# Optimization experiments

Measured on AMD Instinct MI355X. Metric: run time of the kernel, lower is better.

The kernel has to match this reference:

```python
import jax, jax.numpy as jnp
import numpy as np

B, S, D, H, DFF = 8, 1024, 1024, 16, 4096
DK = D // H
NEG = -1000000000.0


def layernorm(x, g, b, eps=1e-5):
    mu = jnp.mean(x, axis=-1, keepdims=True)
    var = jnp.mean((x - mu) ** 2, axis=-1, keepdims=True)
    return (x - mu) / jnp.sqrt(var + eps) * g + b


def setup_inputs() -> dict:
    key = jax.random.key(0)
    ks = jax.random.split(key, 16)
    s = 0.02
    inp = {
        "x": jax.random.normal(ks[0], (B, S, D), jnp.float32),
        "binary_mask": jax.random.randint(ks[1], (B, S), 0, 2, jnp.int32),
        # per-head projections stacked: [H, D, DK]
        "Wq": jax.random.normal(ks[2], (H, D, DK), jnp.float32) * s,
        "bq": jnp.zeros((H, DK), jnp.float32),
        "Wk": jax.random.normal(ks[3], (H, D, DK), jnp.float32) * s,
        "bk": jnp.zeros((H, DK), jnp.float32),
        "Wv": jax.random.normal(ks[4], (H, D, DK), jnp.float32) * s,
        "bv": jnp.zeros((H, DK), jnp.float32),
        "Wo": jax.random.normal(ks[5], (D, D), jnp.float32) * s,
        "bo": jnp.zeros((D,), jnp.float32),
        "ga": jnp.ones((D,), jnp.float32),
        "ba": jnp.zeros((D,), jnp.float32),
        "W1": jax.random.normal(ks[6], (D, DFF), jnp.float32) * s,
        "b1": jnp.zeros((DFF,), jnp.float32),
        "W2": jax.random.normal(ks[7], (DFF, D), jnp.float32) * s,
        "b2": jnp.zeros((D,), jnp.float32),
        "gf": jnp.ones((D,), jnp.float32),
        "bf": jnp.zeros((D,), jnp.float32),
    }
    return inp


def encoder_fwd(x, binary_mask, Wq, bq, Wk, bk, Wv, bv, Wo, bo, ga, ba, W1, b1, W2, b2, gf, bf):
    # --- multi-head self-attention (heads vectorized over h axis) ---
    q = jnp.einsum("bsd,hdk->bhsk", x, Wq) + bq[None, :, None, :]
    k = jnp.einsum("bsd,hdk->bhsk", x, Wk) + bk[None, :, None, :]
    v = jnp.einsum("bsd,hdk->bhsk", x, Wv) + bv[None, :, None, :]
    score = jnp.einsum("bhik,bhjk->bhij", q, k) / jnp.sqrt(jnp.float32(DK))
    # mask: binary_mask is over KEY positions, broadcast over query dim
    score = score + jnp.where(binary_mask[:, None, None, :] == 0, NEG, 0.0)
    # NOTE: original code softmaxes over dim=1 of [B,Sq,Sk] -> the QUERY axis
    probs = jax.nn.softmax(score, axis=2)
    ctx = jnp.einsum("bhij,bhjk->bhik", probs, v)  # [B,H,S,DK]
    ctx = jnp.transpose(ctx, (0, 2, 1, 3)).reshape(x.shape[0], x.shape[1], D)
    attn_out = ctx @ Wo + bo
    y = layernorm(x + attn_out, ga, ba)
    # --- FFN ---
    h = jax.nn.relu(y @ W1 + b1)
    ffn_out = h @ W2 + b2
    return layernorm(y + ffn_out, gf, bf)


def reference(x, binary_mask, Wq, bq, Wk, bk, Wv, bv, Wo, bo, ga, ba, W1, b1, W2, b2, gf, bf):
    return encoder_fwd(x, binary_mask, Wq, bq, Wk, bk, Wv, bv, Wo, bo, ga, ba, W1, b1, W2, b2, gf, bf)
```

## Files before the change

kernel.cpp:

```cpp
#include <hip/hip_runtime.h>
#include <hip/hip_bf16.h>

typedef __bf16 bf16;
typedef __bf16 bf16x8 __attribute__((ext_vector_type(8)));
typedef __bf16 bf16x4 __attribute__((ext_vector_type(4)));
typedef float  f32x4  __attribute__((ext_vector_type(4)));

#define NB 8
#define NS 1024
#define ND 1024
#define NH 16
#define NDK 64
#define NDFF 4096
#define LDT 72
#define LDP 40

static __device__ __forceinline__ f32x4 mfma16(bf16x8 a, bf16x8 b, f32x4 c) {
    return __builtin_amdgcn_mfma_f32_16x16x32_bf16(a, b, c, 0, 0, 0);
}

#define GLDS(g, l) __builtin_amdgcn_global_load_lds( \
    (const __attribute__((address_space(1))) void*)(g), \
    (__attribute__((address_space(3))) void*)(l), 16, 0, 0)

__global__ __launch_bounds__(256) void cvt_x(const float* __restrict__ in,
                                             bf16* __restrict__ out, int n4)
{
    int idx = blockIdx.x * 256 + threadIdx.x;
    if (idx >= n4) return;
    float4 v = ((const float4*)in)[idx];
    bf16x4 o = { (bf16)v.x, (bf16)v.y, (bf16)v.z, (bf16)v.w };
    ((bf16x4*)out)[idx] = o;
}

__global__ __launch_bounds__(256) void prep_transpose(
    const float* __restrict__ Wq, const float* __restrict__ Wk, const float* __restrict__ Wv,
    const float* __restrict__ Wo, const float* __restrict__ W1, const float* __restrict__ W2,
    bf16* __restrict__ wqkvT, bf16* __restrict__ WoT,
    bf16* __restrict__ W1T, bf16* __restrict__ W2T)
{
    __shared__ float T[64][65];
    int bid = blockIdx.x;
    const float* src; bf16* dst; int srcLd, dstLd, tR, tC; bool scale = false;
    if (bid < 768) {
        int mat = bid >> 4, ty = bid & 15;
        int h = mat & 15, type = mat >> 4;
        const float* W = (type == 0) ? Wq : (type == 1 ? Wk : Wv);
        src = W + (size_t)h * ND * NDK;
        srcLd = NDK; tR = ty * 64; tC = 0;
        dst = wqkvT + ((size_t)type * 1024 + h * 64) * ND;
        dstLd = ND;
        scale = (type == 0);
    } else if (bid < 1024) {
        int b2 = bid - 768; int ty = b2 >> 4, tx = b2 & 15;
        src = Wo; srcLd = ND; tR = ty * 64; tC = tx * 64; dst = WoT; dstLd = ND;
    } else if (bid < 2048) {
        int b2 = bid - 1024; int ty = b2 >> 6, tx = b2 & 63;
        src = W1; srcLd = NDFF; tR = ty * 64; tC = tx * 64; dst = W1T; dstLd = ND;
    } else {
        int b2 = bid - 2048; int ty = b2 >> 4, tx = b2 & 15;
        src = W2; srcLd = ND; tR = ty * 64; tC = tx * 64; dst = W2T; dstLd = NDFF;
    }
    int t = threadIdx.x;
    int c0 = t & 63, r0 = t >> 6;
    #pragma unroll
    for (int rr = 0; rr < 16; rr++) {
        int row = rr * 4 + r0;
        T[row][c0] = src[(size_t)(tR + row) * srcLd + tC + c0];
    }
    __syncthreads();
    #pragma unroll
    for (int cc = 0; cc < 16; cc++) {
        int col = cc * 4 + r0;
        float v = T[c0][col];
        if (scale) v *= 0.125f;
        dst[(size_t)(tC + col) * dstLd + tR + c0] = (bf16)v;
    }
}

__global__ void prep_bias(const float* __restrict__ bq, const float* __restrict__ bk,
                          const float* __restrict__ bv, float* __restrict__ bqkv)
{
    int n = blockIdx.x * 256 + threadIdx.x;
    if (n >= 3072) return;
    int type = n >> 10, hk = n & 1023;
    const float* bb = (type == 0) ? bq : (type == 1 ? bk : bv);
    float v = bb[hk];
    if (type == 0) v *= 0.125f;
    bqkv[n] = v;
}

__device__ __forceinline__ void gemm_bt_core(
    const bf16* __restrict__ A, const bf16* __restrict__ BT, int K,
    int rowBase, int colBase, f32x4 (&acc)[4][4], bf16* As, bf16* Bs)
{
    const int tid = threadIdx.x;
    const int lane = tid & 63, wid = tid >> 6;
    const int wr = (wid >> 1) * 64, wc = (wid & 1) * 64;
    const int lrow = lane & 15, lq = lane >> 4;
    const int srow = wid * 32 + (lane >> 3);
    const int gblk = (lane & 7) ^ ((lane >> 3) & 7);
    const bf16* Arow = A + (size_t)(rowBase + srow) * K + gblk * 8;
    const bf16* Brow = BT + (size_t)(colBase + srow) * K + gblk * 8;
    const int co0 = ((lq) ^ (lrow & 7)) * 8;
    const int co1 = ((4 + lq) ^ (lrow & 7)) * 8;
    f32x4 zz = {0.f, 0.f, 0.f, 0.f};
    #pragma unroll
    for (int i = 0; i < 4; i++)
        #pragma unroll
        for (int j = 0; j < 4; j++) acc[i][j] = zz;
    for (int k0 = 0; k0 < K; k0 += 64) {
        __syncthreads();
        #pragma unroll
        for (int it = 0; it < 4; it++)
            GLDS(Arow + (size_t)it * 8 * K + k0, As + (wid * 32 + it * 8) * 64);
        #pragma unroll
        for (int it = 0; it < 4; it++)
            GLDS(Brow + (size_t)it * 8 * K + k0, Bs + (wid * 32 + it * 8) * 64);
        __syncthreads();
        #pragma unroll
        for (int kh = 0; kh < 2; kh++) {
            const int co = kh ? co1 : co0;
            bf16x8 af[4], bfr[4];
            #pragma unroll
            for (int tt = 0; tt < 4; tt++) {
                af[tt]  = *(const bf16x8*)&As[(wr + tt * 16 + lrow) * 64 + co];
                bfr[tt] = *(const bf16x8*)&Bs[(wc + tt * 16 + lrow) * 64 + co];
            }
            #pragma unroll
            for (int i = 0; i < 4; i++)
                #pragma unroll
                for (int j = 0; j < 4; j++)
                    acc[i][j] = mfma16(af[i], bfr[j], acc[i][j]);
        }
    }
}

__global__ __launch_bounds__(256) void g1_qkv(
    const bf16* __restrict__ x, const bf16* __restrict__ wqkvT, const float* __restrict__ bqkv,
    bf16* __restrict__ Q, bf16* __restrict__ Kb, bf16* __restrict__ Vt)
{
    __shared__ bf16 As[128 * 64], Bs[128 * 64];
    f32x4 acc[4][4];
    int rowBase = blockIdx.x * 128, colBase = blockIdx.y * 128;
    gemm_bt_core(x, wqkvT, ND, rowBase, colBase, acc, As, Bs);
    const int tid = threadIdx.x, lane = tid & 63, wid = tid >> 6;
    const int wr = (wid >> 1) * 64, wc = (wid & 1) * 64, lrow = lane & 15, lq = lane >> 4;
    #pragma unroll
    for (int j = 0; j < 4; j++) {
        int gcol = colBase + wc + j * 16 + lrow;
        float bias = bqkv[gcol];
        int type = gcol >> 10, h = (gcol >> 6) & 15, kk = gcol & 63;
        #pragma unroll
        for (int i = 0; i < 4; i++) {
            #pragma unroll
            for (int r = 0; r < 4; r++) {
                int grow = rowBase + wr + i * 16 + lq * 4 + r;
                int b = grow >> 10, s = grow & 1023;
                int bh = b * NH + h;
                bf16 val = (bf16)(acc[i][j][r] + bias);
                if (type == 0)      Q [((size_t)bh * NS + s) * NDK + kk] = val;
                else if (type == 1) Kb[((size_t)bh * NS + s) * NDK + kk] = val;
                else                Vt[((size_t)bh * NDK + kk) * NS + s] = val;
            }
        }
    }
}

__global__ __launch_bounds__(256) void g2_stats(
    const bf16* __restrict__ Q, const bf16* __restrict__ Kb,
    const int* __restrict__ mask, float* __restrict__ alpha)
{
    __shared__ bf16 Ks[128 * LDT];
    __shared__ bf16 Qs[32 * LDT];
    int bh = blockIdx.y, b = bh >> 4;
    int jBase = blockIdx.x * 128;
    const bf16* Kp = Kb + (size_t)bh * NS * NDK;
    const bf16* Qp = Q + (size_t)bh * NS * NDK;
    const int tid = threadIdx.x, lane = tid & 63, wid = tid >> 6;
    const int lrow = lane & 15, lq = lane >> 4, wj = wid * 32;
    #pragma unroll
    for (int c = 0; c < 4; c++) {
        int g = tid + c * 256, row = g >> 3, kc = (g & 7) * 8;
        *(bf16x8*)&Ks[row * LDT + kc] = *(const bf16x8*)&Kp[(size_t)(jBase + row) * NDK + kc];
    }
    float Lacc[2][4];
    #pragma unroll
    for (int jt = 0; jt < 2; jt++)
        #pragma unroll
        for (int r = 0; r < 4; r++) Lacc[jt][r] = 0.f;
    for (int i0 = 0; i0 < NS; i0 += 32) {
        __syncthreads();
        {
            int row = tid >> 3, kc = (tid & 7) * 8;
            *(bf16x8*)&Qs[row * LDT + kc] = *(const bf16x8*)&Qp[(size_t)(i0 + row) * NDK + kc];
        }
        __syncthreads();
        bf16x8 af[2][2], bq8[2][2];
        #pragma unroll
        for (int jt = 0; jt < 2; jt++)
            #pragma unroll
            for (int kh = 0; kh < 2; kh++)
                af[jt][kh] = *(const bf16x8*)&Ks[(wj + jt * 16 + lrow) * LDT + kh * 32 + lq * 8];
        #pragma unroll
        for (int it = 0; it < 2; it++)
            #pragma unroll
            for (int kh = 0; kh < 2; kh++)
                bq8[it][kh] = *(const bf16x8*)&Qs[(it * 16 + lrow) * LDT + kh * 32 + lq * 8];
        #pragma unroll
        for (int jt = 0; jt < 2; jt++) {
            #pragma unroll
            for (int it = 0; it < 2; it++) {
                f32x4 s = {0.f, 0.f, 0.f, 0.f};
                s = mfma16(af[jt][0], bq8[it][0], s);
                s = mfma16(af[jt][1], bq8[it][1], s);
                #pragma unroll
                for (int r = 0; r < 4; r++) Lacc[jt][r] += __expf(s[r]);
            }
        }
    }
    #pragma unroll
    for (int jt = 0; jt < 2; jt++) {
        #pragma unroll
        for (int r = 0; r < 4; r++) {
            float v = Lacc[jt][r];
            v += __shfl_xor(v, 1); v += __shfl_xor(v, 2);
            v += __shfl_xor(v, 4); v += __shfl_xor(v, 8);
            if (lrow == 0) {
                int j = jBase + wj + jt * 16 + lq * 4 + r;
                alpha[(size_t)bh * NS + j] = mask[b * NS + j] ? 1.f / v : 0.f;
            }
        }
    }
}

__global__ __launch_bounds__(256) void kc_cmask(
    const bf16* __restrict__ Vt, const int* __restrict__ mask, float* __restrict__ cmask)
{
    int bh = blockIdx.x, b = bh >> 4;
    int tid = threadIdx.x;
    int kk = tid & 63, part = tid >> 6;
    const bf16* vrow = Vt + ((size_t)bh * NDK + kk) * NS;
    float s = 0.f;
    for (int j = part * 256; j < part * 256 + 256; j++)
        if (mask[b * NS + j] == 0) s += (float)vrow[j];
    __shared__ float red[256];
    red[tid] = s;
    __syncthreads();
    if (part == 0) {
        float t = red[kk] + red[kk + 64] + red[kk + 128] + red[kk + 192];
        cmask[bh * NDK + kk] = t * (1.f / 1024.f);
    }
}

__global__ __launch_bounds__(256) void g3_ctx(
    const bf16* __restrict__ Q, const bf16* __restrict__ Kb, const bf16* __restrict__ Vt,
    const float* __restrict__ alpha, const float* __restrict__ cmask, bf16* __restrict__ ctx)
{
    __shared__ bf16 Qs[128 * LDT];
    __shared__ bf16 Ks[32 * LDT];
    __shared__ bf16 Vs[64 * LDP];
    __shared__ bf16 Ps[4 * 32 * LDP];
    int bh = blockIdx.y, iBase = blockIdx.x * 128;
    int b = bh >> 4, h = bh & 15;
    const bf16* Qp = Q + (size_t)bh * NS * NDK;
    const bf16* Kp = Kb + (size_t)bh * NS * NDK;
    const bf16* Vp = Vt + (size_t)bh * NDK * NS;
    const float* al = alpha + (size_t)bh * NS;
    const int tid = threadIdx.x, lane = tid & 63, wid = tid >> 6;
    const int lrow = lane & 15, lq = lane >> 4, wi = wid * 32;
    #pragma unroll
    for (int c = 0; c < 4; c++) {
        int g = tid + c * 256, row = g >> 3, kc = (g & 7) * 8;
        *(bf16x8*)&Qs[row * LDT + kc] = *(const bf16x8*)&Qp[(size_t)(iBase + row) * NDK + kc];
    }
    f32x4 cacc[2][4];
    f32x4 zz = {0.f, 0.f, 0.f, 0.f};
    #pragma unroll
    for (int it = 0; it < 2; it++)
        #pragma unroll
        for (int kt = 0; kt < 4; kt++) cacc[it][kt] = zz;
    bf16* Pw = Ps + wid * 32 * LDP;
    for (int j0 = 0; j0 < NS; j0 += 32) {
        __syncthreads();
        {
            int row = tid >> 3, kc = (tid & 7) * 8;
            *(bf16x8*)&Ks[row * LDT + kc] = *(const bf16x8*)&Kp[(size_t)(j0 + row) * NDK + kc];
        }
        {
            int kk = tid >> 2, ch = (tid & 3) * 8;
            *(bf16x8*)&Vs[kk * LDP + ch] = *(const bf16x8*)&Vp[(size_t)kk * NS + j0 + ch];
        }
        __syncthreads();
        bf16x8 qa[2][2], kb8[2][2];
        #pragma unroll
        for (int it = 0; it < 2; it++)
            #pragma unroll
            for (int kh = 0; kh < 2; kh++)
                qa[it][kh] = *(const bf16x8*)&Qs[(wi + it * 16 + lrow) * LDT + kh * 32 + lq * 8];
        #pragma unroll
        for (int jt = 0; jt < 2; jt++)
            #pragma unroll
            for (int kh = 0; kh < 2; kh++)
                kb8[jt][kh] = *(const bf16x8*)&Ks[(jt * 16 + lrow) * LDT + kh * 32 + lq * 8];
        float aj0 = al[j0 + lrow];
        float aj1 = al[j0 + 16 + lrow];
        #pragma unroll
        for (int it = 0; it < 2; it++) {
            #pragma unroll
            for (int jt = 0; jt < 2; jt++) {
                f32x4 s = {0.f, 0.f, 0.f, 0.f};
                s = mfma16(qa[it][0], kb8[jt][0], s);
                s = mfma16(qa[it][1], kb8[jt][1], s);
                float aj = jt ? aj1 : aj0;
                #pragma unroll
                for (int r = 0; r < 4; r++) {
                    float p = aj * __expf(s[r]);
                    Pw[(it * 16 + lq * 4 + r) * LDP + jt * 16 + lrow] = (bf16)p;
                }
            }
        }
        __syncthreads();
        bf16x8 pa[2], vb[4];
        #pragma unroll
        for (int it = 0; it < 2; it++)
            pa[it] = *(const bf16x8*)&Pw[(it * 16 + lrow) * LDP + lq * 8];
        #pragma unroll
        for (int kt = 0; kt < 4; kt++)
            vb[kt] = *(const bf16x8*)&Vs[(kt * 16 + lrow) * LDP + lq * 8];
        #pragma unroll
        for (int it = 0; it < 2; it++)
            #pragma unroll
            for (int kt = 0; kt < 4; kt++)
                cacc[it][kt] = mfma16(pa[it], vb[kt], cacc[it][kt]);
    }
    #pragma unroll
    for (int kt = 0; kt < 4; kt++) {
        float cm = cmask[bh * NDK + kt * 16 + lrow];
        int col = h * NDK + kt * 16 + lrow;
        #pragma unroll
        for (int it = 0; it < 2; it++) {
            #pragma unroll
            for (int r = 0; r < 4; r++) {
                int i = iBase + wi + it * 16 + lq * 4 + r;
                ctx[(size_t)(b * NS + i) * ND + col] = (bf16)(cacc[it][kt][r] + cm);
            }
        }
    }
}

__global__ __launch_bounds__(256) void g4_proj(
    const bf16* __restrict__ ctx, const bf16* __restrict__ WoT, const float* __restrict__ bo,
    const float* __restrict__ x, float* __restrict__ t1f)
{
    __shared__ bf16 As[128 * 64], Bs[128 * 64];
    f32x4 acc[4][4];
    int rowBase = blockIdx.x * 128, colBase = blockIdx.y * 128;
    gemm_bt_core(ctx, WoT, ND, rowBase, colBase, acc, As, Bs);
    const int tid = threadIdx.x, lane = tid & 63, wid = tid >> 6;
    const int wr = (wid >> 1) * 64, wc = (wid & 1) * 64, lrow = lane & 15, lq = lane >> 4;
    #pragma unroll
    for (int j = 0; j < 4; j++) {
        int gcol = colBase + wc + j * 16 + lrow;
        float bias = bo[gcol];
        #pragma unroll
        for (int i = 0; i < 4; i++) {
            #pragma unroll
            for (int r = 0; r < 4; r++) {
                int grow = rowBase + wr + i * 16 + lq * 4 + r;
                float v = acc[i][j][r] + bias + x[(size_t)grow * ND + gcol];
                t1f[(size_t)grow * ND + gcol] = v;
            }
        }
    }
}

__global__ __launch_bounds__(256) void g5_ffn1(
    const bf16* __restrict__ y, const bf16* __restrict__ W1T, const float* __restrict__ b1,
    bf16* __restrict__ hb)
{
    __shared__ bf16 As[128 * 64], Bs[128 * 64];
    f32x4 acc[4][4];
    int rowBase = blockIdx.x * 128, colBase = blockIdx.y * 128;
    gemm_bt_core(y, W1T, ND, rowBase, colBase, acc, As, Bs);
    const int tid = threadIdx.x, lane = tid & 63, wid = tid >> 6;
    const int wr = (wid >> 1) * 64, wc = (wid & 1) * 64, lrow = lane & 15, lq = lane >> 4;
    #pragma unroll
    for (int j = 0; j < 4; j++) {
        int gcol = colBase + wc + j * 16 + lrow;
        float bias = b1[gcol];
        #pragma unroll
        for (int i = 0; i < 4; i++) {
            #pragma unroll
            for (int r = 0; r < 4; r++) {
                int grow = rowBase + wr + i * 16 + lq * 4 + r;
                float v = fmaxf(acc[i][j][r] + bias, 0.f);
                hb[(size_t)grow * NDFF + gcol] = (bf16)v;
            }
        }
    }
}

__global__ __launch_bounds__(256) void g6_ffn2(
    const bf16* __restrict__ hb, const bf16* __restrict__ W2T, const float* __restrict__ b2,
    const float* __restrict__ yf, float* __restrict__ zf)
{
    __shared__ bf16 As[128 * 64], Bs[128 * 64];
    f32x4 acc[4][4];
    int rowBase = blockIdx.x * 128, colBase = blockIdx.y * 128;
    gemm_bt_core(hb, W2T, NDFF, rowBase, colBase, acc, As, Bs);
    const int tid = threadIdx.x, lane = tid & 63, wid = tid >> 6;
    const int wr = (wid >> 1) * 64, wc = (wid & 1) * 64, lrow = lane & 15, lq = lane >> 4;
    #pragma unroll
    for (int j = 0; j < 4; j++) {
        int gcol = colBase + wc + j * 16 + lrow;
        float bias = b2[gcol];
        #pragma unroll
        for (int i = 0; i < 4; i++) {
            #pragma unroll
            for (int r = 0; r < 4; r++) {
                int grow = rowBase + wr + i * 16 + lq * 4 + r;
                float v = acc[i][j][r] + bias + yf[(size_t)grow * ND + gcol];
                zf[(size_t)grow * ND + gcol] = v;
            }
        }
    }
}

__global__ __launch_bounds__(256) void ln_kernel(
    const float* __restrict__ in, float* __restrict__ outf, bf16* __restrict__ outb,
    const float* __restrict__ g, const float* __restrict__ bb)
{
    int row = blockIdx.x, tid = threadIdx.x;
    const float* p = in + (size_t)row * ND;
    float4 v4 = ((const float4*)p)[tid];
    float s = v4.x + v4.y + v4.z + v4.w;
    float q = v4.x * v4.x + v4.y * v4.y + v4.z * v4.z + v4.w * v4.w;
    #pragma unroll
    for (int m = 1; m < 64; m <<= 1) { s += __shfl_xor(s, m); q += __shfl_xor(q, m); }
    __shared__ float rs[4], rq[4];
    int wid = tid >> 6, lane = tid & 63;
    if (lane == 0) { rs[wid] = s; rq[wid] = q; }
    __syncthreads();
    s = rs[0] + rs[1] + rs[2] + rs[3];
    q = rq[0] + rq[1] + rq[2] + rq[3];
    float mean = s * (1.f / 1024.f);
    float var = q * (1.f / 1024.f) - mean * mean;
    float rstd = 1.f / sqrtf(var + 1e-5f);
    float vv[4] = {v4.x, v4.y, v4.z, v4.w};
    float4 of;
    bf16x4 ob;
    #pragma unroll
    for (int k = 0; k < 4; k++) {
        int col = tid * 4 + k;
        float yv = (vv[k] - mean) * rstd * g[col] + bb[col];
        ((float*)&of)[k] = yv;
        ob[k] = (bf16)yv;
    }
    ((float4*)(outf + (size_t)row * ND))[tid] = of;
    if (outb) *(bf16x4*)&outb[(size_t)row * ND + tid * 4] = ob;
}

extern "C" void kernel_launch(void* const* d_in, const int* in_sizes, int n_in,
                              void* d_out, int out_size, void* d_ws, size_t ws_size,
                              hipStream_t stream)
{
    const float* x    = (const float*)d_in[0];
    const int*   mask = (const int*)d_in[1];
    const float* Wq   = (const float*)d_in[2];
    const float* bq   = (const float*)d_in[3];
    const float* Wk   = (const float*)d_in[4];
    const float* bk   = (const float*)d_in[5];
    const float* Wv   = (const float*)d_in[6];
    const float* bv   = (const float*)d_in[7];
    const float* Wo   = (const float*)d_in[8];
    const float* bo   = (const float*)d_in[9];
    const float* ga   = (const float*)d_in[10];
    const float* ba   = (const float*)d_in[11];
    const float* W1   = (const float*)d_in[12];
    const float* b1   = (const float*)d_in[13];
    const float* W2   = (const float*)d_in[14];
    const float* b2   = (const float*)d_in[15];
    const float* gf   = (const float*)d_in[16];
    const float* bfb  = (const float*)d_in[17];

    size_t off = 0;
    auto alloc = [&](size_t n) { char* p = (char*)d_ws + off; off += (n + 255) & ~(size_t)255; return (void*)p; };
    bf16*  wqkvT = (bf16*) alloc((size_t)3072 * 1024 * 2);
    bf16*  WoT   = (bf16*) alloc((size_t)1024 * 1024 * 2);
    bf16*  W1T   = (bf16*) alloc((size_t)4096 * 1024 * 2);
    bf16*  W2T   = (bf16*) alloc((size_t)1024 * 4096 * 2);
    float* bqkv  = (float*)alloc(3072 * 4);
    float* alpha = (float*)alloc((size_t)NB * NH * NS * 4);
    float* cmask = (float*)alloc((size_t)NB * NH * NDK * 4);
    bf16*  xb    = (bf16*) alloc((size_t)8192 * 1024 * 2);
    bf16*  ub    = (bf16*) alloc((size_t)8192 * 4096 * 2);
    bf16*  Qb    = ub;
    bf16*  Kb    = ub + (size_t)8192 * 1024;
    bf16*  Vt    = ub + (size_t)2 * 8192 * 1024;
    bf16*  ctx   = ub + (size_t)3 * 8192 * 1024;
    bf16*  hb    = ub;
    float* t1f   = (float*)alloc((size_t)8192 * 1024 * 4);
    float* zf    = t1f;
    bf16*  yb    = (bf16*) alloc((size_t)8192 * 1024 * 2);
    float* yf    = (float*)alloc((size_t)8192 * 1024 * 4);

    cvt_x<<<8192, 256, 0, stream>>>(x, xb, 8192 * 1024 / 4);
    prep_transpose<<<3072, 256, 0, stream>>>(Wq, Wk, Wv, Wo, W1, W2, wqkvT, WoT, W1T, W2T);
    prep_bias<<<12, 256, 0, stream>>>(bq, bk, bv, bqkv);
    g1_qkv<<<dim3(64, 24), 256, 0, stream>>>(xb, wqkvT, bqkv, Qb, Kb, Vt);
    g2_stats<<<dim3(8, 128), 256, 0, stream>>>(Qb, Kb, mask, alpha);
    kc_cmask<<<128, 256, 0, stream>>>(Vt, mask, cmask);
    g3_ctx<<<dim3(8, 128), 256, 0, stream>>>(Qb, Kb, Vt, alpha, cmask, ctx);
    g4_proj<<<dim3(64, 8), 256, 0, stream>>>(ctx, WoT, bo, x, t1f);
    ln_kernel<<<8192, 256, 0, stream>>>(t1f, yf, yb, ga, ba);
    g5_ffn1<<<dim3(64, 32), 256, 0, stream>>>(yb, W1T, b1, hb);
    g6_ffn2<<<dim3(64, 8), 256, 0, stream>>>(hb, W2T, b2, yf, zf);
    ln_kernel<<<8192, 256, 0, stream>>>(zf, (float*)d_out, nullptr, gf, bfb);
}
```

Measured before the change: 576.1 us.

## Restructure attention kernels with swizzled LDS, register-resident Q/K, and a separate V transpose

The QKV GEMM now writes V row-major into a scratch buffer, and a new vt_trans kernel transposes it through LDS with coalesced stores. This replaces the strided scattered Vt writes in the GEMM epilogue. The stats and context kernels keep K (respectively Q) fragments in registers and load the streaming operand with global_load_lds into XOR-swizzled unpadded LDS tiles. They now step 64 keys per iteration, which means fewer barriers and larger MFMA tiles per wave. The masked-key column-mean correction is folded into the probabilities as an additive term packed with alpha in a float2, so the kc_cmask kernel is removed. The cost is an extra launch and extra traffic for the transpose, plus reuse of the t1f buffer as V scratch.

```diff
diff --git a/kernel.cpp b/kernel.cpp
--- a/kernel.cpp
+++ b/kernel.cpp
@@ -12,8 +12,6 @@
 #define NH 16
 #define NDK 64
 #define NDFF 4096
-#define LDT 72
-#define LDP 40
 
 static __device__ __forceinline__ f32x4 mfma16(bf16x8 a, bf16x8 b, f32x4 c) {
     return __builtin_amdgcn_mfma_f32_16x16x32_bf16(a, b, c, 0, 0, 0);
@@ -138,7 +136,7 @@
 
 __global__ __launch_bounds__(256) void g1_qkv(
     const bf16* __restrict__ x, const bf16* __restrict__ wqkvT, const float* __restrict__ bqkv,
-    bf16* __restrict__ Q, bf16* __restrict__ Kb, bf16* __restrict__ Vt)
+    bf16* __restrict__ Q, bf16* __restrict__ Kb, bf16* __restrict__ Vb)
 {
     __shared__ bf16 As[128 * 64], Bs[128 * 64];
     f32x4 acc[4][4];
@@ -151,6 +149,7 @@
         int gcol = colBase + wc + j * 16 + lrow;
         float bias = bqkv[gcol];
         int type = gcol >> 10, h = (gcol >> 6) & 15, kk = gcol & 63;
+        bf16* dst = (type == 0) ? Q : (type == 1 ? Kb : Vb);
         #pragma unroll
         for (int i = 0; i < 4; i++) {
             #pragma unroll
@@ -158,62 +157,79 @@
                 int grow = rowBase + wr + i * 16 + lq * 4 + r;
                 int b = grow >> 10, s = grow & 1023;
                 int bh = b * NH + h;
-                bf16 val = (bf16)(acc[i][j][r] + bias);
-                if (type == 0)      Q [((size_t)bh * NS + s) * NDK + kk] = val;
-                else if (type == 1) Kb[((size_t)bh * NS + s) * NDK + kk] = val;
-                else                Vt[((size_t)bh * NDK + kk) * NS + s] = val;
-            }
-        }
+                dst[((size_t)bh * NS + s) * NDK + kk] = (bf16)(acc[i][j][r] + bias);
+            }
+        }
+    }
+}
+
+__global__ __launch_bounds__(256) void vt_trans(
+    const bf16* __restrict__ Vb, bf16* __restrict__ Vt)
+{
+    __shared__ bf16 T[64 * 72];
+    int bh = blockIdx.y, s0 = blockIdx.x * 64;
+    const bf16* src = Vb + ((size_t)bh * NS + s0) * NDK;
+    int tid = threadIdx.x;
+    #pragma unroll
+    for (int it = 0; it < 2; it++) {
+        int g = tid + it * 256;
+        int row = g >> 3, c = (g & 7) * 8;
+        *(bf16x8*)&T[row * 72 + c] = *(const bf16x8*)&src[row * NDK + c];
+    }
+    __syncthreads();
+    #pragma unroll
+    for (int it = 0; it < 2; it++) {
+        int g = tid + it * 256;
+        int kk = g >> 3, sc = (g & 7) * 8;
+        bf16x8 v;
+        #pragma unroll
+        for (int t = 0; t < 8; t++) v[t] = T[(sc + t) * 72 + kk];
+        *(bf16x8*)&Vt[((size_t)bh * NDK + kk) * NS + s0 + sc] = v;
     }
 }
 
 __global__ __launch_bounds__(256) void g2_stats(
     const bf16* __restrict__ Q, const bf16* __restrict__ Kb,
-    const int* __restrict__ mask, float* __restrict__ alpha)
-{
-    __shared__ bf16 Ks[128 * LDT];
-    __shared__ bf16 Qs[32 * LDT];
+    const int* __restrict__ mask, float2* __restrict__ alpha)
+{
+    __shared__ bf16 Qs[64 * 64];
     int bh = blockIdx.y, b = bh >> 4;
     int jBase = blockIdx.x * 128;
     const bf16* Kp = Kb + (size_t)bh * NS * NDK;
     const bf16* Qp = Q + (size_t)bh * NS * NDK;
     const int tid = threadIdx.x, lane = tid & 63, wid = tid >> 6;
-    const int lrow = lane & 15, lq = lane >> 4, wj = wid * 32;
-    #pragma unroll
-    for (int c = 0; c < 4; c++) {
-        int g = tid + c * 256, row = g >> 3, kc = (g & 7) * 8;
-        *(bf16x8*)&Ks[row * LDT + kc] = *(const bf16x8*)&Kp[(size_t)(jBase + row) * NDK + kc];
-    }
+    const int lrow = lane & 15, lq = lane >> 4;
+    bf16x8 kf[2][2];
+    #pragma unroll
+    for (int jt = 0; jt < 2; jt++)
+        #pragma unroll
+        for (int kh = 0; kh < 2; kh++)
+            kf[jt][kh] = *(const bf16x8*)&Kp[(size_t)(jBase + wid * 32 + jt * 16 + lrow) * NDK + kh * 32 + lq * 8];
+    const int srow = lane >> 3;
+    const int gblk = (lane & 7) ^ srow;
     float Lacc[2][4];
     #pragma unroll
     for (int jt = 0; jt < 2; jt++)
         #pragma unroll
         for (int r = 0; r < 4; r++) Lacc[jt][r] = 0.f;
-    for (int i0 = 0; i0 < NS; i0 += 32) {
-        __syncthreads();
-        {
-            int row = tid >> 3, kc = (tid & 7) * 8;
-            *(bf16x8*)&Qs[row * LDT + kc] = *(const bf16x8*)&Qp[(size_t)(i0 + row) * NDK + kc];
-        }
-        __syncthreads();
-        bf16x8 af[2][2], bq8[2][2];
-        #pragma unroll
-        for (int jt = 0; jt < 2; jt++)
+    f32x4 zz = {0.f, 0.f, 0.f, 0.f};
+    for (int i0 = 0; i0 < NS; i0 += 64) {
+        __syncthreads();
+        #pragma unroll
+        for (int it = 0; it < 2; it++)
+            GLDS(Qp + (size_t)(i0 + wid * 16 + it * 8 + srow) * NDK + gblk * 8,
+                 Qs + (wid * 16 + it * 8) * 64);
+        __syncthreads();
+        #pragma unroll
+        for (int it = 0; it < 4; it++) {
+            bf16x8 qb[2];
             #pragma unroll
             for (int kh = 0; kh < 2; kh++)
-                af[jt][kh] = *(const bf16x8*)&Ks[(wj + jt * 16 + lrow) * LDT + kh * 32 + lq * 8];
-        #pragma unroll
-        for (int it = 0; it < 2; it++)
-            #pragma unroll
-            for (int kh = 0; kh < 2; kh++)
-                bq8[it][kh] = *(const bf16x8*)&Qs[(it * 16 + lrow) * LDT + kh * 32 + lq * 8];
-        #pragma unroll
-        for (int jt = 0; jt < 2; jt++) {
-            #pragma unroll
-            for (int it = 0; it < 2; it++) {
-                f32x4 s = {0.f, 0.f, 0.f, 0.f};
-                s = mfma16(af[jt][0], bq8[it][0], s);
-                s = mfma16(af[jt][1], bq8[it][1], s);
+                qb[kh] = *(const bf16x8*)&Qs[(it * 16 + lrow) * 64 + ((kh * 4 + lq) ^ (lrow & 7)) * 8];
+            #pragma unroll
+            for (int jt = 0; jt < 2; jt++) {
+                f32x4 s = mfma16(kf[jt][0], qb[0], zz);
+                s = mfma16(kf[jt][1], qb[1], s);
                 #pragma unroll
                 for (int r = 0; r < 4; r++) Lacc[jt][r] += __expf(s[r]);
             }
@@ -227,123 +243,111 @@
             v += __shfl_xor(v, 1); v += __shfl_xor(v, 2);
             v += __shfl_xor(v, 4); v += __shfl_xor(v, 8);
             if (lrow == 0) {
-                int j = jBase + wj + jt * 16 + lq * 4 + r;
-                alpha[(size_t)bh * NS + j] = mask[b * NS + j] ? 1.f / v : 0.f;
-            }
-        }
-    }
-}
-
-__global__ __launch_bounds__(256) void kc_cmask(
-    const bf16* __restrict__ Vt, const int* __restrict__ mask, float* __restrict__ cmask)
-{
-    int bh = blockIdx.x, b = bh >> 4;
-    int tid = threadIdx.x;
-    int kk = tid & 63, part = tid >> 6;
-    const bf16* vrow = Vt + ((size_t)bh * NDK + kk) * NS;
-    float s = 0.f;
-    for (int j = part * 256; j < part * 256 + 256; j++)
-        if (mask[b * NS + j] == 0) s += (float)vrow[j];
-    __shared__ float red[256];
-    red[tid] = s;
-    __syncthreads();
-    if (part == 0) {
-        float t = red[kk] + red[kk + 64] + red[kk + 128] + red[kk + 192];
-        cmask[bh * NDK + kk] = t * (1.f / 1024.f);
+                int j = jBase + wid * 32 + jt * 16 + lq * 4 + r;
+                int m = mask[b * NS + j];
+                float2 ac;
+                ac.x = m ? 1.f / v : 0.f;
+                ac.y = m ? 0.f : (1.f / 1024.f);
+                alpha[(size_t)bh * NS + j] = ac;
+            }
+        }
     }
 }
 
 __global__ __launch_bounds__(256) void g3_ctx(
     const bf16* __restrict__ Q, const bf16* __restrict__ Kb, const bf16* __restrict__ Vt,
-    const float* __restrict__ alpha, const float* __restrict__ cmask, bf16* __restrict__ ctx)
-{
-    __shared__ bf16 Qs[128 * LDT];
-    __shared__ bf16 Ks[32 * LDT];
-    __shared__ bf16 Vs[64 * LDP];
-    __shared__ bf16 Ps[4 * 32 * LDP];
+    const float2* __restrict__ alpha, bf16* __restrict__ ctx)
+{
+    __shared__ bf16 Ks[64 * 64];
+    __shared__ bf16 Vs[64 * 64];
+    __shared__ bf16 Ps[128 * 64];
     int bh = blockIdx.y, iBase = blockIdx.x * 128;
     int b = bh >> 4, h = bh & 15;
     const bf16* Qp = Q + (size_t)bh * NS * NDK;
     const bf16* Kp = Kb + (size_t)bh * NS * NDK;
     const bf16* Vp = Vt + (size_t)bh * NDK * NS;
-    const float* al = alpha + (size_t)bh * NS;
+    const float2* al = alpha + (size_t)bh * NS;
     const int tid = threadIdx.x, lane = tid & 63, wid = tid >> 6;
-    const int lrow = lane & 15, lq = lane >> 4, wi = wid * 32;
-    #pragma unroll
-    for (int c = 0; c < 4; c++) {
-        int g = tid + c * 256, row = g >> 3, kc = (g & 7) * 8;
-        *(bf16x8*)&Qs[row * LDT + kc] = *(const bf16x8*)&Qp[(size_t)(iBase + row) * NDK + kc];
-    }
-    f32x4 cacc[2][4];
+    const int lrow = lane & 15, lq = lane >> 4;
+    const int wi = wid >> 1, wsub = wid & 1;
+    bf16x8 qf[4][2];
+    #pragma unroll
+    for (int it = 0; it < 4; it++)
+        #pragma unroll
+        for (int kh = 0; kh < 2; kh++)
+            qf[it][kh] = *(const bf16x8*)&Qp[(size_t)(iBase + wi * 64 + it * 16 + lrow) * NDK + kh * 32 + lq * 8];
+    const int srow = lane >> 3;
+    const int gblk = (lane & 7) ^ srow;
+    f32x4 cacc[4][2];
     f32x4 zz = {0.f, 0.f, 0.f, 0.f};
     #pragma unroll
-    for (int it = 0; it < 2; it++)
-        #pragma unroll
-        for (int kt = 0; kt < 4; kt++) cacc[it][kt] = zz;
-    bf16* Pw = Ps + wid * 32 * LDP;
-    for (int j0 = 0; j0 < NS; j0 += 32) {
-        __syncthreads();
-        {
-            int row = tid >> 3, kc = (tid & 7) * 8;
-            *(bf16x8*)&Ks[row * LDT + kc] = *(const bf16x8*)&Kp[(size_t)(j0 + row) * NDK + kc];
-        }
-        {
-            int kk = tid >> 2, ch = (tid & 3) * 8;
-            *(bf16x8*)&Vs[kk * LDP + ch] = *(const bf16x8*)&Vp[(size_t)kk * NS + j0 + ch];
-        }
-        __syncthreads();
-        bf16x8 qa[2][2], kb8[2][2];
+    for (int it = 0; it < 4; it++)
+        #pragma unroll
+        for (int kt = 0; kt < 2; kt++) cacc[it][kt] = zz;
+    for (int j0 = 0; j0 < NS; j0 += 64) {
+        __syncthreads();
         #pragma unroll
         for (int it = 0; it < 2; it++)
+            GLDS(Kp + (size_t)(j0 + wid * 16 + it * 8 + srow) * NDK + gblk * 8,
+                 Ks + (wid * 16 + it * 8) * 64);
+        #pragma unroll
+        for (int it = 0; it < 2; it++)
+            GLDS(Vp + (size_t)(wid * 16 + it * 8 + srow) * NS + j0 + gblk * 8,
+                 Vs + (wid * 16 + it * 8) * 64);
+        __syncthreads();
+        bf16x8 kb[2][2];
+        #pragma unroll
+        for (int jt = 0; jt < 2; jt++)
             #pragma unroll
             for (int kh = 0; kh < 2; kh++)
-                qa[it][kh] = *(const bf16x8*)&Qs[(wi + it * 16 + lrow) * LDT + kh * 32 + lq * 8];
-        #pragma unroll
-        for (int jt = 0; jt < 2; jt++)
-            #pragma unroll
-            for (int kh = 0; kh < 2; kh++)
-                kb8[jt][kh] = *(const bf16x8*)&Ks[(jt * 16 + lrow) * LDT + kh * 32 + lq * 8];
-        float aj0 = al[j0 + lrow];
-        float aj1 = al[j0 + 16 + lrow];
-        #pragma unroll
-        for (int it = 0; it < 2; it++) {
+                kb[jt][kh] = *(const bf16x8*)&Ks[(wsub * 32 + jt * 16 + lrow) * 64 + ((kh * 4 + lq) ^ (lrow & 7)) * 8];
+        float2 ac[2];
+        ac[0] = al[j0 + wsub * 32 + lrow];
+        ac[1] = al[j0 + wsub * 32 + 16 + lrow];
+        #pragma unroll
+        for (int it = 0; it < 4; it++) {
             #pragma unroll
             for (int jt = 0; jt < 2; jt++) {
-                f32x4 s = {0.f, 0.f, 0.f, 0.f};
-                s = mfma16(qa[it][0], kb8[jt][0], s);
-                s = mfma16(qa[it][1], kb8[jt][1], s);
-                float aj = jt ? aj1 : aj0;
+                f32x4 s = mfma16(qf[it][0], kb[jt][0], zz);
+                s = mfma16(qf[it][1], kb[jt][1], s);
                 #pragma unroll
                 for (int r = 0; r < 4; r++) {
-                    float p = aj * __expf(s[r]);
-                    Pw[(it * 16 + lq * 4 + r) * LDP + jt * 16 + lrow] = (bf16)p;
+                    float p = ac[jt].x * __expf(s[r]) + ac[jt].y;
+                    int i = wi * 64 + it * 16 + lq * 4 + r;
+                    int j = wsub * 32 + jt * 16 + lrow;
+                    Ps[i * 64 + (((j >> 3) ^ (i & 7)) * 8) + (j & 7)] = (bf16)p;
                 }
             }
         }
         __syncthreads();
-        bf16x8 pa[2], vb[4];
-        #pragma unroll
-        for (int it = 0; it < 2; it++)
-            pa[it] = *(const bf16x8*)&Pw[(it * 16 + lrow) * LDP + lq * 8];
-        #pragma unroll
-        for (int kt = 0; kt < 4; kt++)
-            vb[kt] = *(const bf16x8*)&Vs[(kt * 16 + lrow) * LDP + lq * 8];
-        #pragma unroll
-        for (int it = 0; it < 2; it++)
-            #pragma unroll
-            for (int kt = 0; kt < 4; kt++)
-                cacc[it][kt] = mfma16(pa[it], vb[kt], cacc[it][kt]);
-    }
-    #pragma unroll
-    for (int kt = 0; kt < 4; kt++) {
-        float cm = cmask[bh * NDK + kt * 16 + lrow];
-        int col = h * NDK + kt * 16 + lrow;
-        #pragma unroll
-        for (int it = 0; it < 2; it++) {
+        bf16x8 vb[2][2];
+        #pragma unroll
+        for (int kt = 0; kt < 2; kt++)
+            #pragma unroll
+            for (int kh = 0; kh < 2; kh++)
+                vb[kt][kh] = *(const bf16x8*)&Vs[(wsub * 32 + kt * 16 + lrow) * 64 + ((kh * 4 + lq) ^ (lrow & 7)) * 8];
+        #pragma unroll
+        for (int it = 0; it < 4; it++) {
+            bf16x8 pa[2];
+            #pragma unroll
+            for (int kh = 0; kh < 2; kh++)
+                pa[kh] = *(const bf16x8*)&Ps[(wi * 64 + it * 16 + lrow) * 64 + ((kh * 4 + lq) ^ (lrow & 7)) * 8];
+            #pragma unroll
+            for (int kt = 0; kt < 2; kt++) {
+                cacc[it][kt] = mfma16(pa[0], vb[kt][0], cacc[it][kt]);
+                cacc[it][kt] = mfma16(pa[1], vb[kt][1], cacc[it][kt]);
+            }
+        }
+    }
+    #pragma unroll
+    for (int kt = 0; kt < 2; kt++) {
+        int col = h * NDK + wsub * 32 + kt * 16 + lrow;
+        #pragma unroll
+        for (int it = 0; it < 4; it++) {
             #pragma unroll
             for (int r = 0; r < 4; r++) {
-                int i = iBase + wi + it * 16 + lq * 4 + r;
-                ctx[(size_t)(b * NS + i) * ND + col] = (bf16)(cacc[it][kt][r] + cm);
+                int i = iBase + wi * 64 + it * 16 + lq * 4 + r;
+                ctx[(size_t)(b * NS + i) * ND + col] = (bf16)cacc[it][kt][r];
             }
         }
     }
@@ -486,32 +490,32 @@
 
     size_t off = 0;
     auto alloc = [&](size_t n) { char* p = (char*)d_ws + off; off += (n + 255) & ~(size_t)255; return (void*)p; };
-    bf16*  wqkvT = (bf16*) alloc((size_t)3072 * 1024 * 2);
-    bf16*  WoT   = (bf16*) alloc((size_t)1024 * 1024 * 2);
-    bf16*  W1T   = (bf16*) alloc((size_t)4096 * 1024 * 2);
-    bf16*  W2T   = (bf16*) alloc((size_t)1024 * 4096 * 2);
-    float* bqkv  = (float*)alloc(3072 * 4);
-    float* alpha = (float*)alloc((size_t)NB * NH * NS * 4);
-    float* cmask = (float*)alloc((size_t)NB * NH * NDK * 4);
-    bf16*  xb    = (bf16*) alloc((size_t)8192 * 1024 * 2);
-    bf16*  ub    = (bf16*) alloc((size_t)8192 * 4096 * 2);
-    bf16*  Qb    = ub;
-    bf16*  Kb    = ub + (size_t)8192 * 1024;
-    bf16*  Vt    = ub + (size_t)2 * 8192 * 1024;
-    bf16*  ctx   = ub + (size_t)3 * 8192 * 1024;
-    bf16*  hb    = ub;
-    float* t1f   = (float*)alloc((size_t)8192 * 1024 * 4);
-    float* zf    = t1f;
-    bf16*  yb    = (bf16*) alloc((size_t)8192 * 1024 * 2);
-    float* yf    = (float*)alloc((size_t)8192 * 1024 * 4);
+    bf16*   wqkvT = (bf16*)  alloc((size_t)3072 * 1024 * 2);
+    bf16*   WoT   = (bf16*)  alloc((size_t)1024 * 1024 * 2);
+    bf16*   W1T   = (bf16*)  alloc((size_t)4096 * 1024 * 2);
+    bf16*   W2T   = (bf16*)  alloc((size_t)1024 * 4096 * 2);
+    float*  bqkv  = (float*) alloc(3072 * 4);
+    float2* alpha = (float2*)alloc((size_t)NB * NH * NS * 8);
+    bf16*   xb    = (bf16*)  alloc((size_t)8192 * 1024 * 2);
+    bf16*   ub    = (bf16*)  alloc((size_t)8192 * 4096 * 2);
+    bf16*   Qb    = ub;
+    bf16*   Kb    = ub + (size_t)8192 * 1024;
+    bf16*   Vt    = ub + (size_t)2 * 8192 * 1024;
+    bf16*   ctx   = ub + (size_t)3 * 8192 * 1024;
+    bf16*   hb    = ub;
+    float*  t1f   = (float*) alloc((size_t)8192 * 1024 * 4);
+    float*  zf    = t1f;
+    bf16*   Vb    = (bf16*)t1f;
+    bf16*   yb    = (bf16*)  alloc((size_t)8192 * 1024 * 2);
+    float*  yf    = (float*) alloc((size_t)8192 * 1024 * 4);
 
     cvt_x<<<8192, 256, 0, stream>>>(x, xb, 8192 * 1024 / 4);
     prep_transpose<<<3072, 256, 0, stream>>>(Wq, Wk, Wv, Wo, W1, W2, wqkvT, WoT, W1T, W2T);
     prep_bias<<<12, 256, 0, stream>>>(bq, bk, bv, bqkv);
-    g1_qkv<<<dim3(64, 24), 256, 0, stream>>>(xb, wqkvT, bqkv, Qb, Kb, Vt);
+    g1_qkv<<<dim3(64, 24), 256, 0, stream>>>(xb, wqkvT, bqkv, Qb, Kb, Vb);
+    vt_trans<<<dim3(16, 128), 256, 0, stream>>>(Vb, Vt);
     g2_stats<<<dim3(8, 128), 256, 0, stream>>>(Qb, Kb, mask, alpha);
-    kc_cmask<<<128, 256, 0, stream>>>(Vt, mask, cmask);
-    g3_ctx<<<dim3(8, 128), 256, 0, stream>>>(Qb, Kb, Vt, alpha, cmask, ctx);
+    g3_ctx<<<dim3(8, 128), 256, 0, stream>>>(Qb, Kb, Vt, alpha, ctx);
     g4_proj<<<dim3(64, 8), 256, 0, stream>>>(ctx, WoT, bo, x, t1f);
     ln_kernel<<<8192, 256, 0, stream>>>(t1f, yf, yb, ga, ba);
     g5_ffn1<<<dim3(64, 32), 256, 0, stream>>>(yb, W1T, b1, hb);
```

Result: faster. 529.0 us (-8.2%).
